# Performance work log

Hardware: AMD Instinct MI355X
Metric: run time of the kernel (lower is better)

Reference implementation:

```python
import jax, jax.numpy as jnp
import numpy as np

BN_EPS = 1e-5
NN_EPS = 1e-8


def setup_inputs() -> dict:
    key = jax.random.key(0)
    ks = jax.random.split(key, 8)
    B, N, S, D1, D2 = 8, 8192, 2048, 128, 256
    C1, C2 = 256, 128
    Cin = D1 + D2
    return {
        "xyz1": jax.random.normal(ks[0], (B, 3, N), jnp.float32),
        "xyz2": jax.random.normal(ks[1], (B, 3, S), jnp.float32),
        "points1": jax.random.normal(ks[2], (B, D1, N), jnp.float32),
        "points2": jax.random.normal(ks[3], (B, D2, S), jnp.float32),
        "w1": jax.random.normal(ks[4], (C1, Cin), jnp.float32) / np.sqrt(Cin).astype(np.float32),
        "b1": jnp.zeros((C1,), jnp.float32),
        "gamma1": jnp.ones((C1,), jnp.float32),
        "beta1": jnp.zeros((C1,), jnp.float32),
        "w2": jax.random.normal(ks[5], (C2, C1), jnp.float32) / np.sqrt(C1).astype(np.float32),
        "b2": jnp.zeros((C2,), jnp.float32),
        "gamma2": jnp.ones((C2,), jnp.float32),
        "beta2": jnp.zeros((C2,), jnp.float32),
    }


def _three_interpolate(xyz1, xyz2, points2):
    # xyz1: [B,3,N], xyz2: [B,3,S], points2: [B,D2,S] -> [B,D2,N]
    x1 = xyz1.transpose(0, 2, 1)  # [B,N,3]
    x2 = xyz2.transpose(0, 2, 1)  # [B,S,3]
    n1 = jnp.sum(x1 * x1, axis=-1)  # [B,N]
    n2 = jnp.sum(x2 * x2, axis=-1)  # [B,S]
    # squared pairwise distances [B,N,S]
    sqd = n1[:, :, None] + n2[:, None, :] - 2.0 * jnp.einsum("bnc,bsc->bns", x1, x2)
    neg_d, idx = jax.lax.top_k(-sqd, 3)  # 3 nearest neighbors
    dist = -neg_d  # [B,N,3]
    recip = 1.0 / (dist + NN_EPS)
    weight = recip / jnp.sum(recip, axis=-1, keepdims=True)  # [B,N,3]
    p2t = points2.transpose(0, 2, 1)  # [B,S,D2]
    gathered = jax.vmap(lambda p, i: p[i])(p2t, idx)  # [B,N,3,D2]
    return jnp.einsum("bnkd,bnk->bdn", gathered, weight)  # [B,D2,N]


def _conv_bn_relu(x, w, b, gamma, beta):
    # 1x1 Conv1d == channel matmul; BN in training mode (batch stats, biased var)
    x = jnp.einsum("oi,bin->bon", w, x) + b[None, :, None]
    m = jnp.mean(x, axis=(0, 2), keepdims=True)
    v = jnp.var(x, axis=(0, 2), keepdims=True)
    x = (x - m) * jax.lax.rsqrt(v + BN_EPS) * gamma[None, :, None] + beta[None, :, None]
    return jax.nn.relu(x)


def reference(xyz1, xyz2, points1, points2, w1, b1, gamma1, beta1, w2, b2, gamma2, beta2):
    interp = _three_interpolate(xyz1, xyz2, points2)  # [B,D2,N]
    x = jnp.concatenate([points1, interp], axis=1)  # [B,D1+D2,N]
    x = _conv_bn_relu(x, w1, b1, gamma1, beta1)
    x = _conv_bn_relu(x, w2, b2, gamma2, beta2)
    return x
```

## Files before the change

### kernel.cpp

```cpp
#include <hip/hip_runtime.h>
#include <stdint.h>

#define B_   8
#define N_   8192
#define S_   2048
#define D1_  128
#define D2_  256
#define CIN_ 384
#define C1_  256
#define C2_  128
#define NSUB_ 4

typedef uint16_t u16;
typedef uint32_t u32;
typedef __attribute__((ext_vector_type(8))) short bf16x8;
typedef __attribute__((ext_vector_type(4))) float f32x4;

static __device__ __forceinline__ u16 f2bf(float f){
    union { float f; u32 u; } v; v.f = f;
    u32 r = v.u + 0x7FFF + ((v.u >> 16) & 1);
    return (u16)(r >> 16);
}
static __device__ __forceinline__ float bf2f(u16 h){
    union { u32 u; float f; } v; v.u = ((u32)h) << 16;
    return v.f;
}
static __device__ __forceinline__ uint4 pack8(const u16 h[8]){
    uint4 u;
    u.x = (u32)h[0] | ((u32)h[1] << 16);
    u.y = (u32)h[2] | ((u32)h[3] << 16);
    u.z = (u32)h[4] | ((u32)h[5] << 16);
    u.w = (u32)h[6] | ((u32)h[7] << 16);
    return u;
}
#define EXT8(dst, u) { dst[0]=bf2f((u16)(u).x); dst[1]=bf2f((u16)((u).x>>16)); \
                       dst[2]=bf2f((u16)(u).y); dst[3]=bf2f((u16)((u).y>>16)); \
                       dst[4]=bf2f((u16)(u).z); dst[5]=bf2f((u16)((u).z>>16)); \
                       dst[6]=bf2f((u16)(u).w); dst[7]=bf2f((u16)((u).w>>16)); }

static __device__ __forceinline__ float med3f(float a, float b, float c){
    float d;
    asm("v_med3_f32 %0, %1, %2, %3" : "=v"(d) : "v"(a), "v"(b), "v"(c));
    return d;
}

#define INSV(sc) do{ \
    float t2_ = med3f(A1, A2, (sc)); \
    float t1_ = med3f(A0, A1, (sc)); \
    A0 = fmaxf(A0, (sc)); \
    A1 = t1_; A2 = t2_; \
}while(0)
#define INSVB(sc) do{ \
    float t2_ = med3f(Bb1, Bb2, (sc)); \
    float t1_ = med3f(Bb0, Bb1, (sc)); \
    Bb0 = fmaxf(Bb0, (sc)); \
    Bb1 = t1_; Bb2 = t2_; \
}while(0)
#define INSL(sc, si) do{ \
    bool c0 = ((sc) > L0) || ((sc) == L0 && (si) < K0); \
    bool c1 = ((sc) > L1) || ((sc) == L1 && (si) < K1); \
    bool c2 = ((sc) > L2) || ((sc) == L2 && (si) < K2); \
    int K2n = c2 ? (c1 ? K1 : (si)) : K2; \
    int K1n = c1 ? (c0 ? K0 : (si)) : K1; \
    int K0n = c0 ? (si) : K0; \
    float T2 = med3f(L1, L2, (sc)); \
    float T1 = med3f(L0, L1, (sc)); \
    L0 = fmaxf(L0, (sc)); \
    L1 = T1; L2 = T2; K0 = K0n; K1 = K1n; K2 = K2n; \
}while(0)

__global__ __launch_bounds__(256) void k_pre(const float* __restrict__ xyz1,
                                             const float* __restrict__ xyz2,
                                             const float* __restrict__ p2,
                                             const float* __restrict__ w1,
                                             const float* __restrict__ w2,
                                             int4* __restrict__ nn_idx4, float4* __restrict__ nn_w4,
                                             u16* __restrict__ p2t, u16* __restrict__ w1bf,
                                             u16* __restrict__ w2bf){
    __shared__ __attribute__((aligned(16))) char smem[4*513*16];
    int bid = blockIdx.x;
    int t = threadIdx.x;

    if (bid < 1024){
        float4* pt = (float4*)smem;
        int b = bid >> 7;
        int bx = bid & 127;
        const float* xb = xyz2 + (size_t)b*3*S_;
        for (int i = t; i < S_; i += 256){
            float x = xb[i], y = xb[S_ + i], z = xb[2*S_ + i];
            float hw = 0.5f*(x*x + y*y + z*z);
            pt[(i >> 9)*513 + (i & 511)] = make_float4(x, y, z, hw);
        }
        __syncthreads();
        int nl = t >> 2, q = t & 3;
        int n = bx * 64 + nl;
        const float* x1b = xyz1 + (size_t)b*3*N_;
        float px = x1b[n], py = x1b[N_ + n], pz = x1b[2*N_ + n];
        float n1 = px*px + py*py + pz*pz;
        const float4* ptq = pt + q*513;
        const int sQ = q * 512;

        float A0 = -3.4e38f, A1 = -3.4e38f, A2 = -3.4e38f;
        float Bb0 = -3.4e38f, Bb1 = -3.4e38f, Bb2 = -3.4e38f;
        #pragma unroll 4
        for (int j = 0; j < 512; j += 2){
            float4 qa = ptq[j];
            float4 qb = ptq[j+1];
            float sa = fmaf(px, qa.x, fmaf(py, qa.y, fmaf(pz, qa.z, -qa.w)));
            float sb = fmaf(px, qb.x, fmaf(py, qb.y, fmaf(pz, qb.z, -qb.w)));
            INSV(sa);
            INSVB(sb);
        }
        INSV(Bb0); INSV(Bb1); INSV(Bb2);
        const float A0loc = A0;
        #pragma unroll
        for (int m = 1; m <= 2; m <<= 1){
            float e0=__shfl_xor(A0,m), e1=__shfl_xor(A1,m), e2=__shfl_xor(A2,m);
            INSV(e0); INSV(e1); INSV(e2);
        }
        const float M0 = A0, M1 = A1, M2 = A2;

        int i0 = 0x7FFFFFFF, i1 = 0x7FFFFFFF, i2 = 0x7FFFFFFF;
        if (A0loc >= M2){
            #pragma unroll 4
            for (int j = 0; j < 512; ++j){
                float4 qa = ptq[j];
                float sc = fmaf(px, qa.x, fmaf(py, qa.y, fmaf(pz, qa.z, -qa.w)));
                if (__any(sc >= M2)){
                    int sg = sQ + j;
                    i0 = min(i0, sc == M0 ? sg : 0x7FFFFFFF);
                    i1 = min(i1, sc == M1 ? sg : 0x7FFFFFFF);
                    i2 = min(i2, sc == M2 ? sg : 0x7FFFFFFF);
                }
            }
        }
        #pragma unroll
        for (int m = 1; m <= 2; m <<= 1){
            i0 = min(i0, __shfl_xor(i0, m));
            i1 = min(i1, __shfl_xor(i1, m));
            i2 = min(i2, __shfl_xor(i2, m));
        }

        if (M0 == M1 || M1 == M2){
            float L0 = -3.4e38f, L1 = -3.4e38f, L2 = -3.4e38f;
            int K0 = 0x7FFFFFFF, K1 = 0x7FFFFFFF, K2 = 0x7FFFFFFF;
            for (int j = 0; j < 512; ++j){
                float4 qa = ptq[j];
                float sc = fmaf(px, qa.x, fmaf(py, qa.y, fmaf(pz, qa.z, -qa.w)));
                INSL(sc, sQ + j);
            }
            #pragma unroll
            for (int m = 1; m <= 2; m <<= 1){
                float e0=__shfl_xor(L0,m), e1=__shfl_xor(L1,m), e2=__shfl_xor(L2,m);
                int   k0=__shfl_xor(K0,m), k1=__shfl_xor(K1,m), k2=__shfl_xor(K2,m);
                INSL(e0, k0); INSL(e1, k1); INSL(e2, k2);
            }
            i0 = K0; i1 = K1; i2 = K2;
        }

        if (q == 0){
            float d0 = fmaf(-2.f, M0, n1);
            float d1 = fmaf(-2.f, M1, n1);
            float d2 = fmaf(-2.f, M2, n1);
            float r0 = 1.f/(d0+1e-8f), r1 = 1.f/(d1+1e-8f), r2 = 1.f/(d2+1e-8f);
            float inv = 1.f/(r0+r1+r2);
            size_t base = (size_t)b*N_ + n;
            nn_idx4[base] = make_int4(i0, i1, i2, 0);
            nn_w4[base]   = make_float4(r0*inv, r1*inv, r2*inv, 0.f);
        }
    } else if (bid < 1024 + 4096){
        float (*tt)[33] = (float(*)[33])smem;
        int pid = bid - 1024;
        int b = pid >> 9, s0 = (pid & 63) * 32, d0 = ((pid >> 6) & 7) * 32;
        int r = t >> 3, c4 = (t & 7) * 4;
        const float* src = p2 + (((size_t)b*D2_ + d0 + r) * S_ + s0 + c4);
        float4 v = *(const float4*)src;
        tt[r][c4+0]=v.x; tt[r][c4+1]=v.y; tt[r][c4+2]=v.z; tt[r][c4+3]=v.w;
        __syncthreads();
        ushort4 o;
        o.x = f2bf(tt[c4+0][r]); o.y = f2bf(tt[c4+1][r]);
        o.z = f2bf(tt[c4+2][r]); o.w = f2bf(tt[c4+3][r]);
        u16* dst = p2t + (((size_t)b*S_ + s0 + r) * D2_ + d0 + c4);
        *(ushort4*)dst = o;
    } else {
        int i = (bid - 5120) * 256 + t;
        if (i < C1_*CIN_) w1bf[i] = f2bf(w1[i]);
        if (i < C2_*C1_)  w2bf[i] = f2bf(w2[i]);
    }
}

#define SWZ(nrow, kbyte)  ((((nrow)*768 + (kbyte))) ^ (((nrow)&7)<<4))
#define SWZ2(nrow, kbyte) ((((nrow)*512 + (kbyte))) ^ (((nrow)&7)<<4))

__global__ __launch_bounds__(512, 2)
void k_conv1(const u16* __restrict__ w1bf,
    const float* __restrict__ points1, const u16* __restrict__ p2t,
    const int4* __restrict__ nn_idx4, const float4* __restrict__ nn_w4,
    u16* __restrict__ y1, float* __restrict__ part1){
    __shared__ char sm[96*1024];
    int t = threadIdx.x;
    int wave = t >> 6, lane = t & 63;
    int b = blockIdx.y, n0g = blockIdx.x * 128;
    const int nlo = lane & 15, nhi = lane >> 4;
    const int g8 = t & 15, pr = t >> 4;
    const int rb = t >> 3, q8 = t & 7;

    #pragma unroll 1
    for (int sub = 0; sub < 2; ++sub){
        char* X = sm + sub*48*1024;
        float2 va2[8];
        const float* pA = points1 + ((size_t)b*D1_ + g8*8)*N_ + n0g + sub*64 + pr*2;
        #pragma unroll
        for (int j = 0; j < 8; ++j) va2[j] = *(const float2*)(pA + (size_t)j*N_);
        size_t nb = (size_t)b*N_ + n0g + sub*64 + rb;
        int4 nid = nn_idx4[nb];
        float4 nw = nn_w4[nb];
        const u16* r0 = p2t + ((size_t)b*S_ + nid.x)*D2_ + q8*32;
        const u16* r1 = p2t + ((size_t)b*S_ + nid.y)*D2_ + q8*32;
        const u16* r2 = p2t + ((size_t)b*S_ + nid.z)*D2_ + q8*32;
        uint4 uB[12];
        #pragma unroll
        for (int c = 0; c < 4; ++c){
            uB[c]   = *(const uint4*)(r0 + c*8);
            uB[4+c] = *(const uint4*)(r1 + c*8);
            uB[8+c] = *(const uint4*)(r2 + c*8);
        }
        #pragma unroll
        for (int e = 0; e < 2; ++e){
            u16 h[8];
            #pragma unroll
            for (int j = 0; j < 8; ++j) h[j] = f2bf(e ? va2[j].y : va2[j].x);
            *(uint4*)(X + SWZ(pr*2+e, g8*16)) = pack8(h);
        }
        #pragma unroll
        for (int c = 0; c < 4; ++c){
            float f0[8], f1[8], f2v[8];
            EXT8(f0, uB[c]); EXT8(f1, uB[4+c]); EXT8(f2v, uB[8+c]);
            u16 h[8];
            #pragma unroll
            for (int e = 0; e < 8; ++e)
                h[e] = f2bf(fmaf(nw.x, f0[e], fmaf(nw.y, f1[e], nw.z*f2v[e])));
            *(uint4*)(X + SWZ(rb, (128 + q8*32 + c*8)*2)) = pack8(h);
        }
    }
    __syncthreads();

    int blk = blockIdx.y * gridDim.x + blockIdx.x;
    #pragma unroll 1
    for (int pass = 0; pass < 2; ++pass){
        bf16x8 wfr[12];
        {
            const u16* wb = w1bf + ((size_t)(pass*128 + wave*16 + nlo))*CIN_ + nhi*8;
            #pragma unroll
            for (int ks = 0; ks < 12; ++ks) wfr[ks] = *(const bf16x8*)(wb + ks*32);
        }
        float s1a[4] = {0,0,0,0}, s2a[4] = {0,0,0,0};
        #pragma unroll 1
        for (int sub = 0; sub < 2; ++sub){
            char* X = sm + sub*48*1024;
            #pragma unroll 1
            for (int rowg = 0; rowg < 4; ++rowg){
                int nrow = rowg*16 + nlo;
                f32x4 acc = {0.f,0.f,0.f,0.f};
                #pragma unroll
                for (int hf = 0; hf < 2; ++hf){
                    bf16x8 xf[6];
                    #pragma unroll
                    for (int k6 = 0; k6 < 6; ++k6)
                        xf[k6] = *(const bf16x8*)(X + SWZ(nrow, (hf*6+k6)*64 + nhi*16));
                    #pragma unroll
                    for (int k6 = 0; k6 < 6; ++k6)
                        acc = __builtin_amdgcn_mfma_f32_16x16x32_bf16(wfr[hf*6+k6], xf[k6], acc, 0,0,0);
                }
                int n = n0g + sub*64 + nrow;
                u16 h[4];
                #pragma unroll
                for (int r = 0; r < 4; ++r){
                    h[r] = f2bf(acc[r]);
                    s1a[r] += acc[r]; s2a[r] += acc[r]*acc[r];
                }
                uint2 p;
                p.x = (u32)h[0] | ((u32)h[1]<<16); p.y = (u32)h[2] | ((u32)h[3]<<16);
                *(uint2*)(y1 + ((size_t)b*N_ + n)*C1_ + pass*128 + wave*16 + nhi*4) = p;
            }
        }
        #pragma unroll
        for (int r = 0; r < 4; ++r){
            float a = s1a[r], qv = s2a[r];
            #pragma unroll
            for (int m = 1; m <= 8; m <<= 1){ a += __shfl_xor(a, m); qv += __shfl_xor(qv, m); }
            if (nlo == 0){
                int ch = pass*128 + wave*16 + nhi*4 + r;
                part1[(size_t)blk*C1_ + ch] = a;
                part1[(size_t)512*C1_ + (size_t)blk*C1_ + ch] = qv;
            }
        }
    }
}

__global__ __launch_bounds__(512, 2) void k_conv2(const u16* __restrict__ w2bf,
    const u16* __restrict__ y1, const float* __restrict__ a1c1,
    u16* __restrict__ z2bf, float* __restrict__ part2){
    __shared__ char sm[64*1024];
    int t = threadIdx.x;
    int wave = t >> 6, lane = t & 63;
    int b = blockIdx.y, n0g = blockIdx.x * 256;
    const int nlo = lane & 15, nhi = lane >> 4;

    bf16x8 wfr[8];
    {
        const u16* wb = w2bf + ((size_t)(wave*16 + nlo))*C1_ + nhi*8;
        #pragma unroll
        for (int ks = 0; ks < 8; ++ks) wfr[ks] = *(const bf16x8*)(wb + ks*32);
    }

    const int r2 = t >> 4, q16 = t & 15;
    float la8[16], lc8[16];
    {
        const float* ap = a1c1 + q16*16;
        #pragma unroll
        for (int c = 0; c < 4; ++c){
            *(float4*)(la8 + c*4) = *(const float4*)(ap + c*4);
            *(float4*)(lc8 + c*4) = *(const float4*)(ap + 256 + c*4);
        }
    }

    uint4 uy[4];
    auto ISSUE_Y = [&](int s){
        const u16* yp = y1 + ((size_t)b*N_ + n0g + s*64 + r2*2)*C1_ + q16*16;
        #pragma unroll
        for (int e = 0; e < 2; ++e)
            #pragma unroll
            for (int c = 0; c < 2; ++c)
                uy[e*2+c] = *(const uint4*)(yp + (size_t)e*C1_ + c*8);
    };
    auto COMBINE = [&](char* Z){
        #pragma unroll
        for (int e = 0; e < 2; ++e)
            #pragma unroll
            for (int c = 0; c < 2; ++c){
                float f[8]; EXT8(f, uy[e*2+c]);
                u16 h[8];
                #pragma unroll
                for (int k = 0; k < 8; ++k){
                    float z = fmaf(la8[c*8+k], f[k], lc8[c*8+k]);
                    h[k] = f2bf(z > 0.f ? z : 0.f);
                }
                *(uint4*)(Z + SWZ2(r2*2+e, q16*32 + c*16)) = pack8(h);
            }
    };

    char* Zc = sm;
    char* Zn = sm + 32*1024;

    ISSUE_Y(0);
    COMBINE(Zc);
    __syncthreads();

    float s1a[4] = {0,0,0,0}, s2a[4] = {0,0,0,0};
    const int kgB = nhi*16;

    #pragma unroll 1
    for (int s = 0; s < NSUB_; ++s){
        if (s+1 < NSUB_) ISSUE_Y(s+1);
        #pragma unroll
        for (int rowg = 0; rowg < 4; ++rowg){
            int nrow = rowg*16 + nlo;
            f32x4 acc = {0.f,0.f,0.f,0.f};
            #pragma unroll
            for (int hf = 0; hf < 2; ++hf){
                bf16x8 xf[4];
                #pragma unroll
                for (int k4 = 0; k4 < 4; ++k4)
                    xf[k4] = *(const bf16x8*)(Zc + SWZ2(nrow, (hf*4+k4)*64 + kgB));
                #pragma unroll
                for (int k4 = 0; k4 < 4; ++k4)
                    acc = __builtin_amdgcn_mfma_f32_16x16x32_bf16(wfr[hf*4+k4], xf[k4], acc, 0,0,0);
            }
            int n = n0g + s*64 + nrow;
            u16 h[4];
            #pragma unroll
            for (int r = 0; r < 4; ++r){
                h[r] = f2bf(acc[r]);
                s1a[r] += acc[r]; s2a[r] += acc[r]*acc[r];
            }
            uint2 p;
            p.x = (u32)h[0] | ((u32)h[1]<<16); p.y = (u32)h[2] | ((u32)h[3]<<16);
            *(uint2*)(z2bf + ((size_t)b*N_ + n)*C2_ + wave*16 + nhi*4) = p;
        }
        if (s+1 < NSUB_) COMBINE(Zn);
        __syncthreads();
        char* tmp = Zc; Zc = Zn; Zn = tmp;
    }

    int blk = blockIdx.y * gridDim.x + blockIdx.x;
    #pragma unroll
    for (int r = 0; r < 4; ++r){
        float a = s1a[r], qv = s2a[r];
        #pragma unroll
        for (int m = 1; m <= 8; m <<= 1){ a += __shfl_xor(a, m); qv += __shfl_xor(qv, m); }
        if (nlo == 0){
            int ch = wave*16 + nhi*4 + r;
            part2[(size_t)blk*C2_ + ch] = a;
            part2[(size_t)256*C2_ + (size_t)blk*C2_ + ch] = qv;
        }
    }
}

__global__ void k_finalize(const float* __restrict__ part, int C, int NB, float count,
                           const float* __restrict__ gamma, const float* __restrict__ beta,
                           float* __restrict__ ac){
    int o = blockIdx.x, t = threadIdx.x;
    float s1 = 0.f, s2 = 0.f;
    for (int i = t; i < NB; i += 256){
        s1 += part[(size_t)i*C + o];
        s2 += part[(size_t)NB*C + (size_t)i*C + o];
    }
    #pragma unroll
    for (int m = 1; m < 64; m <<= 1){ s1 += __shfl_xor(s1, m); s2 += __shfl_xor(s2, m); }
    __shared__ float ls[8];
    int wave = t >> 6, lane = t & 63;
    if (lane == 0){ ls[wave] = s1; ls[4+wave] = s2; }
    __syncthreads();
    if (t == 0){
        s1 = ls[0]+ls[1]+ls[2]+ls[3];
        s2 = ls[4]+ls[5]+ls[6]+ls[7];
        float mean = s1 / count;
        float var  = s2 / count - mean*mean;
        float inv  = rsqrtf(var + 1e-5f);
        float a = gamma[o] * inv;
        ac[o] = a;
        ac[C + o] = beta[o] - mean*a;
    }
}

__global__ __launch_bounds__(256) void k_apply(const u16* __restrict__ z2bf,
                                               const float* __restrict__ a2c2,
                                               float* __restrict__ out){
    __shared__ float T[128][65];
    __shared__ float la[C2_], lc[C2_];
    int b = blockIdx.y, n0 = blockIdx.x * 64;
    int t = threadIdx.x;
    if (t < C2_){ la[t] = a2c2[t]; lc[t] = a2c2[C2_ + t]; }
    __syncthreads();
    int ck = t & 15, ng = t >> 4;
    #pragma unroll
    for (int g = 0; g < 4; ++g){
        int n = g*16 + ng;
        uint4 v = *(const uint4*)(z2bf + ((size_t)b*N_ + n0 + n)*C2_ + ck*8);
        float f[8]; EXT8(f, v);
        #pragma unroll
        for (int e = 0; e < 8; ++e){
            int ch = ck*8 + e;
            T[ch][n] = fmaxf(fmaf(la[ch], f[e], lc[ch]), 0.f);
        }
    }
    __syncthreads();
    #pragma unroll
    for (int g = 0; g < 8; ++g){
        int id = g*256 + t;
        int ch = id >> 4, f4 = id & 15;
        float4 o;
        o.x = T[ch][f4*4+0]; o.y = T[ch][f4*4+1];
        o.z = T[ch][f4*4+2]; o.w = T[ch][f4*4+3];
        *(float4*)(out + ((size_t)b*C2_ + ch)*N_ + n0 + f4*4) = o;
    }
}

extern "C" void kernel_launch(void* const* d_in, const int* in_sizes, int n_in,
                              void* d_out, int out_size, void* d_ws, size_t ws_size,
                              hipStream_t stream){
    const float* xyz1    = (const float*)d_in[0];
    const float* xyz2    = (const float*)d_in[1];
    const float* points1 = (const float*)d_in[2];
    const float* points2 = (const float*)d_in[3];
    const float* w1      = (const float*)d_in[4];
    const float* gamma1  = (const float*)d_in[6];
    const float* beta1   = (const float*)d_in[7];
    const float* w2      = (const float*)d_in[8];
    const float* gamma2  = (const float*)d_in[10];
    const float* beta2   = (const float*)d_in[11];
    float* outp = (float*)d_out;

    char* ws = (char*)d_ws;
    size_t off = 0;
    auto take = [&](size_t sz) -> void* {
        void* p = ws + off;
        off = (off + sz + 255) & ~(size_t)255;
        return p;
    };
    int4*   nn_idx4 = (int4*)  take((size_t)B_*N_*16);
    float4* nn_w4   = (float4*)take((size_t)B_*N_*16);
    u16*    w1bf    = (u16*)   take((size_t)C1_*CIN_*2);
    u16*    w2bf    = (u16*)   take((size_t)C2_*C1_*2);
    u16*    p2t     = (u16*)   take((size_t)B_*S_*D2_*2);
    u16*    y1      = (u16*)   take((size_t)B_*N_*C1_*2);
    u16*    z2bf    = (u16*)   take((size_t)B_*N_*C2_*2);
    float*  part1   = (float*) take((size_t)2*512*C1_*4);
    float*  part2   = (float*) take((size_t)2*256*C2_*4);
    float*  a1c1    = (float*) take((size_t)2*C1_*4);
    float*  a2c2    = (float*) take((size_t)2*C2_*4);

    hipLaunchKernelGGL(k_pre, dim3(1024 + 4096 + 384), dim3(256), 0, stream,
                       xyz1, xyz2, points2, w1, w2, nn_idx4, nn_w4, p2t, w1bf, w2bf);
    hipLaunchKernelGGL(k_conv1, dim3(N_/128, B_), dim3(512), 0, stream,
                       w1bf, points1, p2t, nn_idx4, nn_w4, y1, part1);
    hipLaunchKernelGGL(k_finalize, dim3(C1_), dim3(256), 0, stream,
                       part1, C1_, 512, (float)(B_*N_), gamma1, beta1, a1c1);
    hipLaunchKernelGGL(k_conv2, dim3(N_/256, B_), dim3(512), 0, stream,
                       w2bf, y1, a1c1, z2bf, part2);
    hipLaunchKernelGGL(k_finalize, dim3(C2_), dim3(256), 0, stream,
                       part2, C2_, 256, (float)(B_*N_), gamma2, beta2, a2c2);
    hipLaunchKernelGGL(k_apply, dim3(N_/64, B_), dim3(256), 0, stream, z2bf, a2c2, outp);
    (void)in_sizes; (void)n_in; (void)out_size; (void)ws_size; (void)d_in;
}
```

Before: 134.5 us.

## Fuse conv1, BN finalize, conv2 and apply into one cooperative persistent kernel

Replaces the five post-processing launches (conv1, two finalize passes, conv2, apply) with a single cooperative kernel of 256 blocks that runs each phase in turn, separated by grid-wide syncs. Blocks loop over tiles in the conv1 and apply phases, and the BN finalize work is spread one channel per block. The aim is to remove per-launch overhead and idle gaps between dependent kernels. In exchange it adds four grid barriers, restricts parallelism to 256 resident blocks, and reads the scale/shift coefficients from global memory in the apply phase instead of from shared memory.

```diff
diff --git a/kernel.cpp b/kernel.cpp
--- a/kernel.cpp
+++ b/kernel.cpp
@@ -1,5 +1,8 @@
 #include <hip/hip_runtime.h>
+#include <hip/hip_cooperative_groups.h>
 #include <stdint.h>
+
+namespace cg = cooperative_groups;
 
 #define B_   8
 #define N_   8192
@@ -192,87 +195,216 @@
 #define SWZ(nrow, kbyte)  ((((nrow)*768 + (kbyte))) ^ (((nrow)&7)<<4))
 #define SWZ2(nrow, kbyte) ((((nrow)*512 + (kbyte))) ^ (((nrow)&7)<<4))
 
-__global__ __launch_bounds__(512, 2)
-void k_conv1(const u16* __restrict__ w1bf,
-    const float* __restrict__ points1, const u16* __restrict__ p2t,
-    const int4* __restrict__ nn_idx4, const float4* __restrict__ nn_w4,
-    u16* __restrict__ y1, float* __restrict__ part1){
-    __shared__ char sm[96*1024];
+__global__ __launch_bounds__(512, 2) void k_post(
+    const u16* __restrict__ w1bf, const float* __restrict__ points1,
+    const u16* __restrict__ p2t, const int4* __restrict__ nn_idx4,
+    const float4* __restrict__ nn_w4, u16* __restrict__ y1, float* __restrict__ part1,
+    const float* __restrict__ gamma1, const float* __restrict__ beta1, float* __restrict__ a1c1,
+    const u16* __restrict__ w2bf, float* __restrict__ part2,
+    const float* __restrict__ gamma2, const float* __restrict__ beta2, float* __restrict__ a2c2,
+    u16* __restrict__ z2bf, float* __restrict__ outp)
+{
+    __shared__ __attribute__((aligned(16))) char sm[96*1024];
+    cg::grid_group gg = cg::this_grid();
     int t = threadIdx.x;
+    int bid = blockIdx.x;
     int wave = t >> 6, lane = t & 63;
-    int b = blockIdx.y, n0g = blockIdx.x * 128;
     const int nlo = lane & 15, nhi = lane >> 4;
-    const int g8 = t & 15, pr = t >> 4;
-    const int rb = t >> 3, q8 = t & 7;
-
-    #pragma unroll 1
-    for (int sub = 0; sub < 2; ++sub){
-        char* X = sm + sub*48*1024;
-        float2 va2[8];
-        const float* pA = points1 + ((size_t)b*D1_ + g8*8)*N_ + n0g + sub*64 + pr*2;
+
+    {
+        const int g8 = t & 15, pr = t >> 4;
+        const int rb = t >> 3, q8 = t & 7;
+        #pragma unroll 1
+        for (int tile = bid; tile < 512; tile += 256){
+            int b = tile >> 6, n0g = (tile & 63) * 128;
+            #pragma unroll 1
+            for (int sub = 0; sub < 2; ++sub){
+                char* X = sm + sub*48*1024;
+                float2 va2[8];
+                const float* pA = points1 + ((size_t)b*D1_ + g8*8)*N_ + n0g + sub*64 + pr*2;
+                #pragma unroll
+                for (int j = 0; j < 8; ++j) va2[j] = *(const float2*)(pA + (size_t)j*N_);
+                size_t nb = (size_t)b*N_ + n0g + sub*64 + rb;
+                int4 nid = nn_idx4[nb];
+                float4 nw = nn_w4[nb];
+                const u16* r0 = p2t + ((size_t)b*S_ + nid.x)*D2_ + q8*32;
+                const u16* r1 = p2t + ((size_t)b*S_ + nid.y)*D2_ + q8*32;
+                const u16* r2 = p2t + ((size_t)b*S_ + nid.z)*D2_ + q8*32;
+                uint4 uB[12];
+                #pragma unroll
+                for (int c = 0; c < 4; ++c){
+                    uB[c]   = *(const uint4*)(r0 + c*8);
+                    uB[4+c] = *(const uint4*)(r1 + c*8);
+                    uB[8+c] = *(const uint4*)(r2 + c*8);
+                }
+                #pragma unroll
+                for (int e = 0; e < 2; ++e){
+                    u16 h[8];
+                    #pragma unroll
+                    for (int j = 0; j < 8; ++j) h[j] = f2bf(e ? va2[j].y : va2[j].x);
+                    *(uint4*)(X + SWZ(pr*2+e, g8*16)) = pack8(h);
+                }
+                #pragma unroll
+                for (int c = 0; c < 4; ++c){
+                    float f0[8], f1[8], f2v[8];
+                    EXT8(f0, uB[c]); EXT8(f1, uB[4+c]); EXT8(f2v, uB[8+c]);
+                    u16 h[8];
+                    #pragma unroll
+                    for (int e = 0; e < 8; ++e)
+                        h[e] = f2bf(fmaf(nw.x, f0[e], fmaf(nw.y, f1[e], nw.z*f2v[e])));
+                    *(uint4*)(X + SWZ(rb, (128 + q8*32 + c*8)*2)) = pack8(h);
+                }
+            }
+            __syncthreads();
+
+            #pragma unroll 1
+            for (int pass = 0; pass < 2; ++pass){
+                bf16x8 wfr[12];
+                {
+                    const u16* wb = w1bf + ((size_t)(pass*128 + wave*16 + nlo))*CIN_ + nhi*8;
+                    #pragma unroll
+                    for (int ks = 0; ks < 12; ++ks) wfr[ks] = *(const bf16x8*)(wb + ks*32);
+                }
+                float s1a[4] = {0,0,0,0}, s2a[4] = {0,0,0,0};
+                #pragma unroll 1
+                for (int sub = 0; sub < 2; ++sub){
+                    char* X = sm + sub*48*1024;
+                    #pragma unroll 1
+                    for (int rowg = 0; rowg < 4; ++rowg){
+                        int nrow = rowg*16 + nlo;
+                        f32x4 acc = {0.f,0.f,0.f,0.f};
+                        #pragma unroll
+                        for (int hf = 0; hf < 2; ++hf){
+                            bf16x8 xf[6];
+                            #pragma unroll
+                            for (int k6 = 0; k6 < 6; ++k6)
+                                xf[k6] = *(const bf16x8*)(X + SWZ(nrow, (hf*6+k6)*64 + nhi*16));
+                            #pragma unroll
+                            for (int k6 = 0; k6 < 6; ++k6)
+                                acc = __builtin_amdgcn_mfma_f32_16x16x32_bf16(wfr[hf*6+k6], xf[k6], acc, 0,0,0);
+                        }
+                        int n = n0g + sub*64 + nrow;
+                        u16 h[4];
+                        #pragma unroll
+                        for (int r = 0; r < 4; ++r){
+                            h[r] = f2bf(acc[r]);
+                            s1a[r] += acc[r]; s2a[r] += acc[r]*acc[r];
+                        }
+                        uint2 p;
+                        p.x = (u32)h[0] | ((u32)h[1]<<16); p.y = (u32)h[2] | ((u32)h[3]<<16);
+                        *(uint2*)(y1 + ((size_t)b*N_ + n)*C1_ + pass*128 + wave*16 + nhi*4) = p;
+                    }
+                }
+                #pragma unroll
+                for (int r = 0; r < 4; ++r){
+                    float a = s1a[r], qv = s2a[r];
+                    #pragma unroll
+                    for (int m = 1; m <= 8; m <<= 1){ a += __shfl_xor(a, m); qv += __shfl_xor(qv, m); }
+                    if (nlo == 0){
+                        int ch = pass*128 + wave*16 + nhi*4 + r;
+                        part1[(size_t)tile*C1_ + ch] = a;
+                        part1[(size_t)512*C1_ + (size_t)tile*C1_ + ch] = qv;
+                    }
+                }
+            }
+            __syncthreads();
+        }
+    }
+    __threadfence();
+    gg.sync();
+
+    {
+        int ch = bid;
+        float s1 = part1[(size_t)t*C1_ + ch];
+        float s2 = part1[(size_t)512*C1_ + (size_t)t*C1_ + ch];
         #pragma unroll
-        for (int j = 0; j < 8; ++j) va2[j] = *(const float2*)(pA + (size_t)j*N_);
-        size_t nb = (size_t)b*N_ + n0g + sub*64 + rb;
-        int4 nid = nn_idx4[nb];
-        float4 nw = nn_w4[nb];
-        const u16* r0 = p2t + ((size_t)b*S_ + nid.x)*D2_ + q8*32;
-        const u16* r1 = p2t + ((size_t)b*S_ + nid.y)*D2_ + q8*32;
-        const u16* r2 = p2t + ((size_t)b*S_ + nid.z)*D2_ + q8*32;
-        uint4 uB[12];
-        #pragma unroll
-        for (int c = 0; c < 4; ++c){
-            uB[c]   = *(const uint4*)(r0 + c*8);
-            uB[4+c] = *(const uint4*)(r1 + c*8);
-            uB[8+c] = *(const uint4*)(r2 + c*8);
-        }
-        #pragma unroll
-        for (int e = 0; e < 2; ++e){
-            u16 h[8];
-            #pragma unroll
-            for (int j = 0; j < 8; ++j) h[j] = f2bf(e ? va2[j].y : va2[j].x);
-            *(uint4*)(X + SWZ(pr*2+e, g8*16)) = pack8(h);
-        }
-        #pragma unroll
-        for (int c = 0; c < 4; ++c){
-            float f0[8], f1[8], f2v[8];
-            EXT8(f0, uB[c]); EXT8(f1, uB[4+c]); EXT8(f2v, uB[8+c]);
-            u16 h[8];
-            #pragma unroll
-            for (int e = 0; e < 8; ++e)
-                h[e] = f2bf(fmaf(nw.x, f0[e], fmaf(nw.y, f1[e], nw.z*f2v[e])));
-            *(uint4*)(X + SWZ(rb, (128 + q8*32 + c*8)*2)) = pack8(h);
-        }
+        for (int m = 1; m < 64; m <<= 1){ s1 += __shfl_xor(s1, m); s2 += __shfl_xor(s2, m); }
+        float* ls = (float*)sm;
+        if (lane == 0){ ls[wave] = s1; ls[8+wave] = s2; }
+        __syncthreads();
+        if (t == 0){
+            s1 = 0.f; s2 = 0.f;
+            #pragma unroll
+            for (int w = 0; w < 8; ++w){ s1 += ls[w]; s2 += ls[8+w]; }
+            float mean = s1 / 65536.f;
+            float var  = s2 / 65536.f - mean*mean;
+            float inv  = rsqrtf(var + 1e-5f);
+            float a = gamma1[ch] * inv;
+            a1c1[ch] = a;
+            a1c1[C1_ + ch] = beta1[ch] - mean*a;
+        }
+        __syncthreads();
     }
-    __syncthreads();
-
-    int blk = blockIdx.y * gridDim.x + blockIdx.x;
-    #pragma unroll 1
-    for (int pass = 0; pass < 2; ++pass){
-        bf16x8 wfr[12];
+    __threadfence();
+    gg.sync();
+
+    {
+        int b = bid >> 5, n0g = (bid & 31) * 256;
+        bf16x8 wfr[8];
         {
-            const u16* wb = w1bf + ((size_t)(pass*128 + wave*16 + nlo))*CIN_ + nhi*8;
-            #pragma unroll
-            for (int ks = 0; ks < 12; ++ks) wfr[ks] = *(const bf16x8*)(wb + ks*32);
-        }
+            const u16* wb = w2bf + ((size_t)(wave*16 + nlo))*C1_ + nhi*8;
+            #pragma unroll
+            for (int ks = 0; ks < 8; ++ks) wfr[ks] = *(const bf16x8*)(wb + ks*32);
+        }
+        const int r2 = t >> 4, q16 = t & 15;
+        float la8[16], lc8[16];
+        {
+            const float* ap = a1c1 + q16*16;
+            #pragma unroll
+            for (int c = 0; c < 4; ++c){
+                *(float4*)(la8 + c*4) = *(const float4*)(ap + c*4);
+                *(float4*)(lc8 + c*4) = *(const float4*)(ap + 256 + c*4);
+            }
+        }
+        uint4 uy[4];
+        auto ISSUE_Y = [&](int s){
+            const u16* yp = y1 + ((size_t)b*N_ + n0g + s*64 + r2*2)*C1_ + q16*16;
+            #pragma unroll
+            for (int e = 0; e < 2; ++e)
+                #pragma unroll
+                for (int c = 0; c < 2; ++c)
+                    uy[e*2+c] = *(const uint4*)(yp + (size_t)e*C1_ + c*8);
+        };
+        auto COMBINE = [&](char* Z){
+            #pragma unroll
+            for (int e = 0; e < 2; ++e)
+                #pragma unroll
+                for (int c = 0; c < 2; ++c){
+                    float f[8]; EXT8(f, uy[e*2+c]);
+                    u16 h[8];
+                    #pragma unroll
+                    for (int k = 0; k < 8; ++k){
+                        float z = fmaf(la8[c*8+k], f[k], lc8[c*8+k]);
+                        h[k] = f2bf(z > 0.f ? z : 0.f);
+                    }
+                    *(uint4*)(Z + SWZ2(r2*2+e, q16*32 + c*16)) = pack8(h);
+                }
+        };
+        char* Zc = sm;
+        char* Zn = sm + 32*1024;
+        ISSUE_Y(0);
+        COMBINE(Zc);
+        __syncthreads();
         float s1a[4] = {0,0,0,0}, s2a[4] = {0,0,0,0};
+        const int kgB = nhi*16;
         #pragma unroll 1
-        for (int sub = 0; sub < 2; ++sub){
-            char* X = sm + sub*48*1024;
-            #pragma unroll 1
+        for (int s = 0; s < NSUB_; ++s){
+            if (s+1 < NSUB_) ISSUE_Y(s+1);
+            #pragma unroll
             for (int rowg = 0; rowg < 4; ++rowg){
                 int nrow = rowg*16 + nlo;
                 f32x4 acc = {0.f,0.f,0.f,0.f};
                 #pragma unroll
                 for (int hf = 0; hf < 2; ++hf){
-                    bf16x8 xf[6];
-                    #pragma unroll
-                    for (int k6 = 0; k6 < 6; ++k6)
-                        xf[k6] = *(const bf16x8*)(X + SWZ(nrow, (hf*6+k6)*64 + nhi*16));
-                    #pragma unroll
-                    for (int k6 = 0; k6 < 6; ++k6)
-                        acc = __builtin_amdgcn_mfma_f32_16x16x32_bf16(wfr[hf*6+k6], xf[k6], acc, 0,0,0);
-                }
-                int n = n0g + sub*64 + nrow;
+                    bf16x8 xf[4];
+                    #pragma unroll
+                    for (int k4 = 0; k4 < 4; ++k4)
+                        xf[k4] = *(const bf16x8*)(Zc + SWZ2(nrow, (hf*4+k4)*64 + kgB));
+                    #pragma unroll
+                    for (int k4 = 0; k4 < 4; ++k4)
+                        acc = __builtin_amdgcn_mfma_f32_16x16x32_bf16(wfr[hf*4+k4], xf[k4], acc, 0,0,0);
+                }
+                int n = n0g + s*64 + nrow;
                 u16 h[4];
                 #pragma unroll
                 for (int r = 0; r < 4; ++r){
@@ -281,8 +413,11 @@
                 }
                 uint2 p;
                 p.x = (u32)h[0] | ((u32)h[1]<<16); p.y = (u32)h[2] | ((u32)h[3]<<16);
-                *(uint2*)(y1 + ((size_t)b*N_ + n)*C1_ + pass*128 + wave*16 + nhi*4) = p;
-            }
+                *(uint2*)(z2bf + ((size_t)b*N_ + n)*C2_ + wave*16 + nhi*4) = p;
+            }
+            if (s+1 < NSUB_) COMBINE(Zn);
+            __syncthreads();
+            char* tmp = Zc; Zc = Zn; Zn = tmp;
         }
         #pragma unroll
         for (int r = 0; r < 4; ++r){
@@ -290,180 +425,70 @@
             #pragma unroll
             for (int m = 1; m <= 8; m <<= 1){ a += __shfl_xor(a, m); qv += __shfl_xor(qv, m); }
             if (nlo == 0){
-                int ch = pass*128 + wave*16 + nhi*4 + r;
-                part1[(size_t)blk*C1_ + ch] = a;
-                part1[(size_t)512*C1_ + (size_t)blk*C1_ + ch] = qv;
+                int ch = wave*16 + nhi*4 + r;
+                part2[(size_t)bid*C2_ + ch] = a;
+                part2[(size_t)256*C2_ + (size_t)bid*C2_ + ch] = qv;
             }
         }
     }
-}
-
-__global__ __launch_bounds__(512, 2) void k_conv2(const u16* __restrict__ w2bf,
-    const u16* __restrict__ y1, const float* __restrict__ a1c1,
-    u16* __restrict__ z2bf, float* __restrict__ part2){
-    __shared__ char sm[64*1024];
-    int t = threadIdx.x;
-    int wave = t >> 6, lane = t & 63;
-    int b = blockIdx.y, n0g = blockIdx.x * 256;
-    const int nlo = lane & 15, nhi = lane >> 4;
-
-    bf16x8 wfr[8];
+    __threadfence();
+    gg.sync();
+
+    if (bid < C2_){
+        int ch = bid;
+        float s1 = (t < 256) ? part2[(size_t)t*C2_ + ch] : 0.f;
+        float s2 = (t < 256) ? part2[(size_t)256*C2_ + (size_t)t*C2_ + ch] : 0.f;
+        #pragma unroll
+        for (int m = 1; m < 64; m <<= 1){ s1 += __shfl_xor(s1, m); s2 += __shfl_xor(s2, m); }
+        float* ls = (float*)sm;
+        if (lane == 0){ ls[wave] = s1; ls[8+wave] = s2; }
+        __syncthreads();
+        if (t == 0){
+            s1 = 0.f; s2 = 0.f;
+            #pragma unroll
+            for (int w = 0; w < 8; ++w){ s1 += ls[w]; s2 += ls[8+w]; }
+            float mean = s1 / 65536.f;
+            float var  = s2 / 65536.f - mean*mean;
+            float inv  = rsqrtf(var + 1e-5f);
+            float a = gamma2[ch] * inv;
+            a2c2[ch] = a;
+            a2c2[C2_ + ch] = beta2[ch] - mean*a;
+        }
+    }
+    __threadfence();
+    gg.sync();
+
     {
-        const u16* wb = w2bf + ((size_t)(wave*16 + nlo))*C1_ + nhi*8;
-        #pragma unroll
-        for (int ks = 0; ks < 8; ++ks) wfr[ks] = *(const bf16x8*)(wb + ks*32);
-    }
-
-    const int r2 = t >> 4, q16 = t & 15;
-    float la8[16], lc8[16];
-    {
-        const float* ap = a1c1 + q16*16;
-        #pragma unroll
-        for (int c = 0; c < 4; ++c){
-            *(float4*)(la8 + c*4) = *(const float4*)(ap + c*4);
-            *(float4*)(lc8 + c*4) = *(const float4*)(ap + 256 + c*4);
-        }
-    }
-
-    uint4 uy[4];
-    auto ISSUE_Y = [&](int s){
-        const u16* yp = y1 + ((size_t)b*N_ + n0g + s*64 + r2*2)*C1_ + q16*16;
-        #pragma unroll
-        for (int e = 0; e < 2; ++e)
-            #pragma unroll
-            for (int c = 0; c < 2; ++c)
-                uy[e*2+c] = *(const uint4*)(yp + (size_t)e*C1_ + c*8);
-    };
-    auto COMBINE = [&](char* Z){
-        #pragma unroll
-        for (int e = 0; e < 2; ++e)
-            #pragma unroll
-            for (int c = 0; c < 2; ++c){
-                float f[8]; EXT8(f, uy[e*2+c]);
-                u16 h[8];
-                #pragma unroll
-                for (int k = 0; k < 8; ++k){
-                    float z = fmaf(la8[c*8+k], f[k], lc8[c*8+k]);
-                    h[k] = f2bf(z > 0.f ? z : 0.f);
-                }
-                *(uint4*)(Z + SWZ2(r2*2+e, q16*32 + c*16)) = pack8(h);
-            }
-    };
-
-    char* Zc = sm;
-    char* Zn = sm + 32*1024;
-
-    ISSUE_Y(0);
-    COMBINE(Zc);
-    __syncthreads();
-
-    float s1a[4] = {0,0,0,0}, s2a[4] = {0,0,0,0};
-    const int kgB = nhi*16;
-
-    #pragma unroll 1
-    for (int s = 0; s < NSUB_; ++s){
-        if (s+1 < NSUB_) ISSUE_Y(s+1);
-        #pragma unroll
-        for (int rowg = 0; rowg < 4; ++rowg){
-            int nrow = rowg*16 + nlo;
-            f32x4 acc = {0.f,0.f,0.f,0.f};
-            #pragma unroll
-            for (int hf = 0; hf < 2; ++hf){
-                bf16x8 xf[4];
-                #pragma unroll
-                for (int k4 = 0; k4 < 4; ++k4)
-                    xf[k4] = *(const bf16x8*)(Zc + SWZ2(nrow, (hf*4+k4)*64 + kgB));
-                #pragma unroll
-                for (int k4 = 0; k4 < 4; ++k4)
-                    acc = __builtin_amdgcn_mfma_f32_16x16x32_bf16(wfr[hf*4+k4], xf[k4], acc, 0,0,0);
-            }
-            int n = n0g + s*64 + nrow;
-            u16 h[4];
-            #pragma unroll
-            for (int r = 0; r < 4; ++r){
-                h[r] = f2bf(acc[r]);
-                s1a[r] += acc[r]; s2a[r] += acc[r]*acc[r];
-            }
-            uint2 p;
-            p.x = (u32)h[0] | ((u32)h[1]<<16); p.y = (u32)h[2] | ((u32)h[3]<<16);
-            *(uint2*)(z2bf + ((size_t)b*N_ + n)*C2_ + wave*16 + nhi*4) = p;
-        }
-        if (s+1 < NSUB_) COMBINE(Zn);
-        __syncthreads();
-        char* tmp = Zc; Zc = Zn; Zn = tmp;
-    }
-
-    int blk = blockIdx.y * gridDim.x + blockIdx.x;
-    #pragma unroll
-    for (int r = 0; r < 4; ++r){
-        float a = s1a[r], qv = s2a[r];
-        #pragma unroll
-        for (int m = 1; m <= 8; m <<= 1){ a += __shfl_xor(a, m); qv += __shfl_xor(qv, m); }
-        if (nlo == 0){
-            int ch = wave*16 + nhi*4 + r;
-            part2[(size_t)blk*C2_ + ch] = a;
-            part2[(size_t)256*C2_ + (size_t)blk*C2_ + ch] = qv;
-        }
-    }
-}
-
-__global__ void k_finalize(const float* __restrict__ part, int C, int NB, float count,
-                           const float* __restrict__ gamma, const float* __restrict__ beta,
-                           float* __restrict__ ac){
-    int o = blockIdx.x, t = threadIdx.x;
-    float s1 = 0.f, s2 = 0.f;
-    for (int i = t; i < NB; i += 256){
-        s1 += part[(size_t)i*C + o];
-        s2 += part[(size_t)NB*C + (size_t)i*C + o];
-    }
-    #pragma unroll
-    for (int m = 1; m < 64; m <<= 1){ s1 += __shfl_xor(s1, m); s2 += __shfl_xor(s2, m); }
-    __shared__ float ls[8];
-    int wave = t >> 6, lane = t & 63;
-    if (lane == 0){ ls[wave] = s1; ls[4+wave] = s2; }
-    __syncthreads();
-    if (t == 0){
-        s1 = ls[0]+ls[1]+ls[2]+ls[3];
-        s2 = ls[4]+ls[5]+ls[6]+ls[7];
-        float mean = s1 / count;
-        float var  = s2 / count - mean*mean;
-        float inv  = rsqrtf(var + 1e-5f);
-        float a = gamma[o] * inv;
-        ac[o] = a;
-        ac[C + o] = beta[o] - mean*a;
-    }
-}
-
-__global__ __launch_bounds__(256) void k_apply(const u16* __restrict__ z2bf,
-                                               const float* __restrict__ a2c2,
-                                               float* __restrict__ out){
-    __shared__ float T[128][65];
-    __shared__ float la[C2_], lc[C2_];
-    int b = blockIdx.y, n0 = blockIdx.x * 64;
-    int t = threadIdx.x;
-    if (t < C2_){ la[t] = a2c2[t]; lc[t] = a2c2[C2_ + t]; }
-    __syncthreads();
-    int ck = t & 15, ng = t >> 4;
-    #pragma unroll
-    for (int g = 0; g < 4; ++g){
-        int n = g*16 + ng;
-        uint4 v = *(const uint4*)(z2bf + ((size_t)b*N_ + n0 + n)*C2_ + ck*8);
-        float f[8]; EXT8(f, v);
-        #pragma unroll
-        for (int e = 0; e < 8; ++e){
-            int ch = ck*8 + e;
-            T[ch][n] = fmaxf(fmaf(la[ch], f[e], lc[ch]), 0.f);
-        }
-    }
-    __syncthreads();
-    #pragma unroll
-    for (int g = 0; g < 8; ++g){
-        int id = g*256 + t;
-        int ch = id >> 4, f4 = id & 15;
-        float4 o;
-        o.x = T[ch][f4*4+0]; o.y = T[ch][f4*4+1];
-        o.z = T[ch][f4*4+2]; o.w = T[ch][f4*4+3];
-        *(float4*)(out + ((size_t)b*C2_ + ch)*N_ + n0 + f4*4) = o;
+        int half = t >> 8, tt = t & 255;
+        float (*T)[65] = (float(*)[65])(sm + half*33280);
+        int ck = tt & 15, ng = tt >> 4;
+        #pragma unroll 1
+        for (int pair = bid; pair < 512; pair += 256){
+            int tile = pair*2 + half;
+            int b = tile >> 7, n0 = (tile & 127) * 64;
+            #pragma unroll
+            for (int g = 0; g < 4; ++g){
+                int n = g*16 + ng;
+                uint4 v = *(const uint4*)(z2bf + ((size_t)b*N_ + n0 + n)*C2_ + ck*8);
+                float f[8]; EXT8(f, v);
+                #pragma unroll
+                for (int e = 0; e < 8; ++e){
+                    int ch = ck*8 + e;
+                    T[ch][n] = fmaxf(fmaf(a2c2[ch], f[e], a2c2[C2_ + ch]), 0.f);
+                }
+            }
+            __syncthreads();
+            #pragma unroll
+            for (int g = 0; g < 8; ++g){
+                int id = g*256 + tt;
+                int ch = id >> 4, f4 = id & 15;
+                float4 o;
+                o.x = T[ch][f4*4+0]; o.y = T[ch][f4*4+1];
+                o.z = T[ch][f4*4+2]; o.w = T[ch][f4*4+3];
+                *(float4*)(outp + ((size_t)b*C2_ + ch)*N_ + n0 + f4*4) = o;
+            }
+            __syncthreads();
+        }
     }
 }
 
@@ -503,14 +528,13 @@
 
     hipLaunchKernelGGL(k_pre, dim3(1024 + 4096 + 384), dim3(256), 0, stream,
                        xyz1, xyz2, points2, w1, w2, nn_idx4, nn_w4, p2t, w1bf, w2bf);
-    hipLaunchKernelGGL(k_conv1, dim3(N_/128, B_), dim3(512), 0, stream,
-                       w1bf, points1, p2t, nn_idx4, nn_w4, y1, part1);
-    hipLaunchKernelGGL(k_finalize, dim3(C1_), dim3(256), 0, stream,
-                       part1, C1_, 512, (float)(B_*N_), gamma1, beta1, a1c1);
-    hipLaunchKernelGGL(k_conv2, dim3(N_/256, B_), dim3(512), 0, stream,
-                       w2bf, y1, a1c1, z2bf, part2);
-    hipLaunchKernelGGL(k_finalize, dim3(C2_), dim3(256), 0, stream,
-                       part2, C2_, 256, (float)(B_*N_), gamma2, beta2, a2c2);
-    hipLaunchKernelGGL(k_apply, dim3(N_/64, B_), dim3(256), 0, stream, z2bf, a2c2, outp);
+
+    void* args[] = {
+        (void*)&w1bf, (void*)&points1, (void*)&p2t, (void*)&nn_idx4, (void*)&nn_w4,
+        (void*)&y1, (void*)&part1, (void*)&gamma1, (void*)&beta1, (void*)&a1c1,
+        (void*)&w2bf, (void*)&part2, (void*)&gamma2, (void*)&beta2, (void*)&a2c2,
+        (void*)&z2bf, (void*)&outp
+    };
+    hipLaunchCooperativeKernel((const void*)k_post, dim3(256), dim3(512), args, 0, stream);
     (void)in_sizes; (void)n_in; (void)out_size; (void)ws_size; (void)d_in;
 }
```

Measured after the change: 386.8 us. +187.6%, slower.
